# Kernel tuning notes

Hardware: AMD Instinct MI355X
Metric: run time of the kernel (lower is better)

The kernel has to match this reference:

```python
import jax, jax.numpy as jnp
import numpy as np

N = 4096
BATCH = 4
NT = 256  # nt from init_kwargs


def setup_inputs() -> dict:
    key = jax.random.key(0)
    k1, k2, k3, k4 = jax.random.split(key, 4)
    scale = 0.05 / np.sqrt(N)  # keep spectral radius << 1 for numerical stability
    B_real = jax.random.normal(k1, (N, N), dtype=jnp.float32) * scale
    B_imag = jax.random.normal(k2, (N, N), dtype=jnp.float32) * scale
    # omega: per-node frequencies, |omega| <= 0.5 so the diagonal part is contractive
    omega = jax.random.uniform(k3, (BATCH, N), dtype=jnp.float32, minval=-0.5, maxval=0.5)
    # initial state on the unit circle: x0 = exp(i * theta), theta in (-pi, pi)
    x0_angles = jax.random.uniform(k4, (BATCH, N), dtype=jnp.float32, minval=-np.pi, maxval=np.pi)
    return {"B_real": B_real, "B_imag": B_imag, "omega": omega, "x0_angles": x0_angles}


def reference(B_real, B_imag, omega, x0_angles):
    B = B_real + 1j * B_imag            # (N, N) complex64
    x0 = jnp.exp(1j * x0_angles)        # (BATCH, N) complex64, unit-circle init

    def step(x, _):
        # x_{t+1} = i*diag(omega) x_t + B x_t  (batched dense matvec)
        x_next = 1j * omega * x + jnp.einsum('mn,bn->bm', B, x)
        return x_next, x_next

    _, hist = jax.lax.scan(step, x0, None, length=NT - 1)
    # (NT, BATCH, N): initial state followed by NT-1 scan outputs
    return jnp.concatenate([x0[None, ...], hist], axis=0)
```

## Files before the change

kernel.cpp:

```cpp
#include <hip/hip_runtime.h>
#include <stdint.h>

#define NN 4096
#define BB 4
#define MROWS 16
#define TPB 512
#define NBLK 256
#define REDS 17
#define RING 16
#define XSZ  (8 * NN)

typedef __attribute__((ext_vector_type(8))) short bf16x8;
typedef __attribute__((ext_vector_type(4))) float f32x4;

__device__ __forceinline__ uint32_t bf16rne(float f) {
  uint32_t u = __float_as_uint(f);
  return (u + 0x7FFFu + ((u >> 16) & 1u)) >> 16;
}

__global__ void pack_planes(const float* __restrict__ Br, const float* __restrict__ Bi,
                            uint4* __restrict__ Brb, uint4* __restrict__ Bib) {
  int i = blockIdx.x * blockDim.x + threadIdx.x;
  const float4* r4 = reinterpret_cast<const float4*>(Br) + (size_t)i * 2;
  const float4* m4 = reinterpret_cast<const float4*>(Bi) + (size_t)i * 2;
  float4 a0 = r4[0], a1 = r4[1];
  float4 b0 = m4[0], b1 = m4[1];
  uint4 o;
  o.x = bf16rne(a0.x) | (bf16rne(a0.y) << 16);
  o.y = bf16rne(a0.z) | (bf16rne(a0.w) << 16);
  o.z = bf16rne(a1.x) | (bf16rne(a1.y) << 16);
  o.w = bf16rne(a1.z) | (bf16rne(a1.w) << 16);
  Brb[i] = o;
  o.x = bf16rne(b0.x) | (bf16rne(b0.y) << 16);
  o.y = bf16rne(b0.z) | (bf16rne(b0.w) << 16);
  o.z = bf16rne(b1.x) | (bf16rne(b1.y) << 16);
  o.w = bf16rne(b1.z) | (bf16rne(b1.w) << 16);
  Bib[i] = o;
}

__global__ __launch_bounds__(TPB)
void rnn_persistent(const uint16_t* __restrict__ Brb,
                    const uint16_t* __restrict__ Bib,
                    const float* __restrict__ omega,
                    const float* __restrict__ ang,
                    uint16_t* __restrict__ xring,
                    uint32_t* __restrict__ flags,
                    float* __restrict__ out,
                    int NT) {
  extern __shared__ char smem[];
  uint4* BrL = (uint4*)smem;
  float* red = (float*)(smem + 131072);

  const int tid  = threadIdx.x;
  const int w    = tid >> 6;
  const int lane = tid & 63;
  const int al   = lane & 15;
  const int kq   = lane >> 4;
  const int row0 = blockIdx.x * MROWS;
  const int bid  = blockIdx.x;
  const int p1   = al & 7;
  const int p2   = p1 ^ 1;
  const int swz  = al & 7;
  const uint64_t sm64 = (al & 1) ? 0ull : 0x8000800080008000ull;

  for (int j = tid; j < MROWS * 512; j += TPB) {
    int row = j >> 9;
    int u   = j & 511;
    uint4 v = *(const uint4*)(Brb + (size_t)(row0 + row) * NN + u * 8);
    BrL[row * 512 + (u ^ (row & 7))] = v;
  }

  float myval = 0.f, om = 0.f;
  int bb = 0, mm = 0, ri = 0, cc = 0;
  if (tid < 128) {
    int r = tid >> 3; cc = tid & 7;
    mm = row0 + r; bb = cc >> 1; ri = cc & 1;
    om = omega[bb * NN + mm];
    float sv, cv;
    sincosf(ang[bb * NN + mm], &sv, &cv);
    myval = ri ? sv : cv;
    if (!ri) out[bb * NN + mm] = myval;
    float s2 = __shfl(myval, (lane + 8) & 63, 64);
    if (!((tid >> 3) & 1)) {
      uint32_t pk = bf16rne(myval) | (bf16rne(s2) << 16);
      uint32_t* dst = (uint32_t*)xring + ((cc * NN + mm) >> 1);
      __hip_atomic_store(dst, pk, __ATOMIC_RELAXED, __HIP_MEMORY_SCOPE_AGENT);
    }
  }
  __syncthreads();
  if (tid == 0)
    __hip_atomic_store(&flags[bid * 16], 1u, __ATOMIC_RELAXED, __HIP_MEMORY_SCOPE_AGENT);

  const int nb = w * 512 + kq * 8;
  const uint16_t* birow = Bib + (size_t)(row0 + al) * NN + nb;

  for (int t = 1; t < NT; ++t) {
    if (tid < 64) {
      const uint32_t want = (uint32_t)t;
      bool done = false;
      for (int spin = 0; spin < (1 << 22) && !done; ++spin) {
        bool ok = true;
#pragma unroll
        for (int i = 0; i < 4; ++i) {
          uint32_t f = __hip_atomic_load(&flags[(lane * 4 + i) * 16],
                                         __ATOMIC_RELAXED, __HIP_MEMORY_SCOPE_AGENT);
          ok &= (f >= want);
        }
        done = (bool)__all(ok);
        if (!done) __builtin_amdgcn_s_sleep(2);
      }
    }
    __syncthreads();

    const uint16_t* xs = xring + (size_t)((t - 1) & (RING - 1)) * XSZ;
    f32x4 accA = {0.f, 0.f, 0.f, 0.f};
    f32x4 accB = {0.f, 0.f, 0.f, 0.f};

#define SSTEP(S)                                                                \
    { union { uint4 q; bf16x8 v; } fr;                                         \
      fr.q = BrL[al * 512 + (((w << 6) + (S << 2) + kq) ^ swz)];                \
      bf16x8 fi = *(const bf16x8*)(birow + S * 32);                            \
      const uint16_t* x1p = xs + p1 * NN + nb + S * 32;                         \
      const uint16_t* x2p = xs + p2 * NN + nb + S * 32;                         \
      union { uint64_t q[2]; bf16x8 v; } u1, u2;                                \
      u1.q[0] = *(const uint64_t*)(x1p);                                        \
      u1.q[1] = *(const uint64_t*)(x1p + 4);                                    \
      u2.q[0] = *(const uint64_t*)(x2p) ^ sm64;                                 \
      u2.q[1] = *(const uint64_t*)(x2p + 4) ^ sm64;                             \
      accA = __builtin_amdgcn_mfma_f32_16x16x32_bf16(fr.v, u1.v, accA, 0, 0, 0);\
      accB = __builtin_amdgcn_mfma_f32_16x16x32_bf16(fi, u2.v, accB, 0, 0, 0); }
    SSTEP(0)  SSTEP(1)  SSTEP(2)  SSTEP(3)
    SSTEP(4)  SSTEP(5)  SSTEP(6)  SSTEP(7)
    SSTEP(8)  SSTEP(9)  SSTEP(10) SSTEP(11)
    SSTEP(12) SSTEP(13) SSTEP(14) SSTEP(15)
#undef SSTEP

    {
      float* rw = red + w * 16 * REDS;
      rw[(kq * 4 + 0) * REDS + al] = accA[0] + accB[0];
      rw[(kq * 4 + 1) * REDS + al] = accA[1] + accB[1];
      rw[(kq * 4 + 2) * REDS + al] = accA[2] + accB[2];
      rw[(kq * 4 + 3) * REDS + al] = accA[3] + accB[3];
    }
    __syncthreads();

    if (tid < 128) {
      int r = tid >> 3;
      float s = 0.f;
#pragma unroll
      for (int w2 = 0; w2 < 8; ++w2) s += red[w2 * 16 * REDS + r * REDS + cc];
      float other = __shfl_xor(myval, 1, 64);
      float xr = ri ? other : myval;
      float xi = ri ? myval : other;
      s += ri ? (om * xr) : (-om * xi);
      myval = s;
      if (!ri) out[(size_t)t * (BB * NN) + bb * NN + mm] = s;
      float s2 = __shfl(s, (lane + 8) & 63, 64);
      if (!((tid >> 3) & 1)) {
        uint32_t pk = bf16rne(s) | (bf16rne(s2) << 16);
        uint32_t* dst = (uint32_t*)(xring + (size_t)(t & (RING - 1)) * XSZ)
                        + ((cc * NN + mm) >> 1);
        __hip_atomic_store(dst, pk, __ATOMIC_RELAXED, __HIP_MEMORY_SCOPE_AGENT);
      }
    }
    __syncthreads();
    if (tid == 0)
      __hip_atomic_store(&flags[bid * 16], (uint32_t)(t + 1),
                         __ATOMIC_RELAXED, __HIP_MEMORY_SCOPE_AGENT);
  }
}

__global__ void init_kernel(const float* __restrict__ ang,
                            float2* __restrict__ st0, float* __restrict__ out0) {
  int i = blockIdx.x * blockDim.x + threadIdx.x;
  if (i < BB * NN) {
    float s, c;
    sincosf(ang[i], &s, &c);
    st0[i] = make_float2(c, s);
    out0[i] = c;
  }
}

__global__ __launch_bounds__(1024)
void step_fb(const float* __restrict__ Brf, const float* __restrict__ Bif,
             const float* __restrict__ omega,
             const float2* __restrict__ stPrev, float2* __restrict__ stNext,
             float* __restrict__ outRe) {
  extern __shared__ float lds[];
  float* xl  = lds;
  float* xh  = lds + NN * 4;
  float* red = lds + NN * 8;
  const int tid = threadIdx.x;
#pragma unroll
  for (int k = 0; k < 8; ++k) {
    int idx = tid + k * 1024;
    int half = idx >> 12;
    int n = idx & (NN - 1);
    float2 v0 = stPrev[(half * 2) * NN + n];
    float2 v1 = stPrev[(half * 2 + 1) * NN + n];
    reinterpret_cast<float4*>(half ? xh : xl)[n] = make_float4(v0.x, v0.y, v1.x, v1.y);
  }
  __syncthreads();
  const int w = tid >> 6, lane = tid & 63, rg = w >> 2, q = w & 3;
  const int row0 = blockIdx.x * MROWS + rg * 4;
  float acc[4][8];
#pragma unroll
  for (int r = 0; r < 4; ++r)
#pragma unroll
    for (int c = 0; c < 8; ++c) acc[r][c] = 0.0f;
#define CFMA(A, BR, BI, XA, XB)                                   \
  A[0] = fmaf(BR, XA.x, A[0]); A[0] = fmaf(-BI, XA.y, A[0]);      \
  A[1] = fmaf(BR, XA.y, A[1]); A[1] = fmaf(BI, XA.x, A[1]);       \
  A[2] = fmaf(BR, XA.z, A[2]); A[2] = fmaf(-BI, XA.w, A[2]);      \
  A[3] = fmaf(BR, XA.w, A[3]); A[3] = fmaf(BI, XA.z, A[3]);       \
  A[4] = fmaf(BR, XB.x, A[4]); A[4] = fmaf(-BI, XB.y, A[4]);      \
  A[5] = fmaf(BR, XB.y, A[5]); A[5] = fmaf(BI, XB.x, A[5]);       \
  A[6] = fmaf(BR, XB.z, A[6]); A[6] = fmaf(-BI, XB.w, A[6]);      \
  A[7] = fmaf(BR, XB.w, A[7]); A[7] = fmaf(BI, XB.z, A[7]);
  for (int i4 = 0; i4 < 4; ++i4) {
    const int n0 = q * 1024 + i4 * 256 + lane * 4;
    float4 xa[4], xb[4];
#pragma unroll
    for (int j = 0; j < 4; ++j) {
      xa[j] = reinterpret_cast<const float4*>(xl)[n0 + j];
      xb[j] = reinterpret_cast<const float4*>(xh)[n0 + j];
    }
#pragma unroll
    for (int r = 0; r < 4; ++r) {
      const float4 pvr = reinterpret_cast<const float4*>(Brf + (size_t)(row0 + r) * NN)[q * 256 + i4 * 64 + lane];
      const float4 pvi = reinterpret_cast<const float4*>(Bif + (size_t)(row0 + r) * NN)[q * 256 + i4 * 64 + lane];
      float* a = acc[r];
      CFMA(a, pvr.x, pvi.x, xa[0], xb[0]);
      CFMA(a, pvr.y, pvi.y, xa[1], xb[1]);
      CFMA(a, pvr.z, pvi.z, xa[2], xb[2]);
      CFMA(a, pvr.w, pvi.w, xa[3], xb[3]);
    }
  }
#undef CFMA
  float t0 = acc[0][0], t1 = acc[0][1], t2 = acc[0][2], t3 = acc[0][3];
  float t4 = acc[0][4], t5 = acc[0][5], t6 = acc[0][6], t7 = acc[0][7];
  float t8 = acc[1][0], t9 = acc[1][1], t10 = acc[1][2], t11 = acc[1][3];
  float t12 = acc[1][4], t13 = acc[1][5], t14 = acc[1][6], t15 = acc[1][7];
  float t16 = acc[2][0], t17 = acc[2][1], t18 = acc[2][2], t19 = acc[2][3];
  float t20 = acc[2][4], t21 = acc[2][5], t22 = acc[2][6], t23 = acc[2][7];
  float t24 = acc[3][0], t25 = acc[3][1], t26 = acc[3][2], t27 = acc[3][3];
  float t28 = acc[3][4], t29 = acc[3][5], t30 = acc[3][6], t31 = acc[3][7];
#define RSTEP(LO, HI, M)                                          \
  { float s_ = up ? LO : HI;                                      \
    s_ = __shfl_xor(s_, M, 64);                                   \
    LO = (up ? HI : LO) + s_; }
  { const bool up = (lane & 32) != 0;
    RSTEP(t0, t16, 32)  RSTEP(t1, t17, 32)  RSTEP(t2, t18, 32)  RSTEP(t3, t19, 32)
    RSTEP(t4, t20, 32)  RSTEP(t5, t21, 32)  RSTEP(t6, t22, 32)  RSTEP(t7, t23, 32)
    RSTEP(t8, t24, 32)  RSTEP(t9, t25, 32)  RSTEP(t10, t26, 32) RSTEP(t11, t27, 32)
    RSTEP(t12, t28, 32) RSTEP(t13, t29, 32) RSTEP(t14, t30, 32) RSTEP(t15, t31, 32) }
  { const bool up = (lane & 16) != 0;
    RSTEP(t0, t8, 16)  RSTEP(t1, t9, 16)  RSTEP(t2, t10, 16) RSTEP(t3, t11, 16)
    RSTEP(t4, t12, 16) RSTEP(t5, t13, 16) RSTEP(t6, t14, 16) RSTEP(t7, t15, 16) }
  { const bool up = (lane & 8) != 0;
    RSTEP(t0, t4, 8) RSTEP(t1, t5, 8) RSTEP(t2, t6, 8) RSTEP(t3, t7, 8) }
  { const bool up = (lane & 4) != 0;
    RSTEP(t0, t2, 4) RSTEP(t1, t3, 4) }
  { const bool up = (lane & 2) != 0;
    RSTEP(t0, t1, 2) }
#undef RSTEP
  t0 += __shfl_xor(t0, 1, 64);
  if (!(lane & 1)) red[w * 32 + ((lane >> 1) & 31)] = t0;
  __syncthreads();
  if (tid < 128) {
    int rg2 = tid >> 5, v = tid & 31;
    float s = red[(rg2 * 4 + 0) * 32 + v] + red[(rg2 * 4 + 1) * 32 + v] +
              red[(rg2 * 4 + 2) * 32 + v] + red[(rg2 * 4 + 3) * 32 + v];
    int r = v >> 3, c = v & 7, b = c >> 1, ri = c & 1;
    int m = blockIdx.x * MROWS + rg2 * 4 + r;
    float om = omega[b * NN + m];
    const float* xs = (b < 2) ? xl : xh;
    float xr = xs[m * 4 + (b & 1) * 2];
    float xi = xs[m * 4 + (b & 1) * 2 + 1];
    s += (ri == 0) ? (-om * xi) : (om * xr);
    reinterpret_cast<float*>(stNext)[(b * NN + m) * 2 + ri] = s;
    if (ri == 0) outRe[b * NN + m] = s;
  }
}

extern "C" void kernel_launch(void* const* d_in, const int* in_sizes, int n_in,
                              void* d_out, int out_size, void* d_ws, size_t ws_size,
                              hipStream_t stream) {
  const float* B_real = (const float*)d_in[0];
  const float* B_imag = (const float*)d_in[1];
  const float* omega  = (const float*)d_in[2];
  const float* ang    = (const float*)d_in[3];
  float* out = (float*)d_out;

  int NT = out_size / (BB * NN);
  const size_t planeBytes = (size_t)NN * NN * 2;
  const size_t xringBytes = (size_t)RING * XSZ * 2;
  const size_t flagBytes  = 256 * 16 * sizeof(uint32_t);
  const bool coop = ws_size >= 2 * planeBytes + xringBytes + flagBytes;

  hipError_t launched = hipErrorUnknown;
  if (coop) {
    uint16_t* Brb   = (uint16_t*)d_ws;
    uint16_t* Bib   = Brb + (size_t)NN * NN;
    uint16_t* xring = (uint16_t*)((char*)d_ws + 2 * planeBytes);
    uint32_t* flags = (uint32_t*)((char*)d_ws + 2 * planeBytes + xringBytes);

    (void)hipMemsetAsync((void*)flags, 0, flagBytes, stream);
    pack_planes<<<NN * NN / 8 / 256, 256, 0, stream>>>(B_real, B_imag,
                                                       (uint4*)Brb, (uint4*)Bib);

    const size_t shmem = 131072 + (size_t)8 * 16 * REDS * 4;
    (void)hipFuncSetAttribute((const void*)&rnn_persistent,
                              hipFuncAttributeMaxDynamicSharedMemorySize, (int)shmem);

    void* kargs[8];
    kargs[0] = (void*)&Brb;
    kargs[1] = (void*)&Bib;
    kargs[2] = (void*)&omega;
    kargs[3] = (void*)&ang;
    kargs[4] = (void*)&xring;
    kargs[5] = (void*)&flags;
    kargs[6] = (void*)&out;
    kargs[7] = (void*)&NT;
    launched = hipLaunchCooperativeKernel((const void*)&rnn_persistent,
                                          dim3(NBLK), dim3(TPB),
                                          kargs, (unsigned int)shmem, stream);
  }

  if (launched != hipSuccess) {
    float2* st0 = (float2*)d_ws;
    float2* st1 = st0 + BB * NN;
    const size_t shmemF = (size_t)(NN * 8 + 16 * 32) * sizeof(float);
    (void)hipFuncSetAttribute((const void*)&step_fb,
                              hipFuncAttributeMaxDynamicSharedMemorySize, (int)shmemF);
    init_kernel<<<(BB * NN + 255) / 256, 256, 0, stream>>>(ang, st0, out);
    for (int t = 1; t < NT; ++t) {
      float2* sp = ((t - 1) & 1) ? st1 : st0;
      float2* sn = (t & 1) ? st1 : st0;
      float* outT = out + (size_t)t * BB * NN;
      step_fb<<<NN / MROWS, 1024, shmemF, stream>>>(B_real, B_imag, omega, sp, sn, outT);
    }
  }
}
```

Measured before the change: 2.363 ms.

## Replace all-to-all flag polling with master-block barrier and epoch broadcast

Per-step grid synchronization changes from every block polling all 256 per-block flags to a two-level scheme. Block 0 waits on all flags, one thread per flag, then publishes an epoch counter, and every other block spins on that single word with one thread. Flags are padded to 128-byte spacing. The aim is to cut global polling traffic and contention on the flag lines, at the cost of an extra serialized hop (gather, then broadcast) in every step's barrier latency.

```diff
diff --git a/kernel.cpp b/kernel.cpp
--- a/kernel.cpp
+++ b/kernel.cpp
@@ -9,6 +9,7 @@
 #define REDS 17
 #define RING 16
 #define XSZ  (8 * NN)
+#define EPOCH_OFF (256 * 32)
 
 typedef __attribute__((ext_vector_type(8))) short bf16x8;
 typedef __attribute__((ext_vector_type(4))) float f32x4;
@@ -89,28 +90,38 @@
   }
   __syncthreads();
   if (tid == 0)
-    __hip_atomic_store(&flags[bid * 16], 1u, __ATOMIC_RELAXED, __HIP_MEMORY_SCOPE_AGENT);
+    __hip_atomic_store(&flags[bid * 32], 1u, __ATOMIC_RELAXED, __HIP_MEMORY_SCOPE_AGENT);
 
   const int nb = w * 512 + kq * 8;
   const uint16_t* birow = Bib + (size_t)(row0 + al) * NN + nb;
 
   for (int t = 1; t < NT; ++t) {
-    if (tid < 64) {
-      const uint32_t want = (uint32_t)t;
-      bool done = false;
-      for (int spin = 0; spin < (1 << 22) && !done; ++spin) {
-        bool ok = true;
-#pragma unroll
-        for (int i = 0; i < 4; ++i) {
-          uint32_t f = __hip_atomic_load(&flags[(lane * 4 + i) * 16],
+    if (bid == 0) {
+      if (tid < 256) {
+        const uint32_t want = (uint32_t)t;
+        for (int spin = 0; spin < (1 << 22); ++spin) {
+          uint32_t f = __hip_atomic_load(&flags[tid * 32],
                                          __ATOMIC_RELAXED, __HIP_MEMORY_SCOPE_AGENT);
-          ok &= (f >= want);
+          if (f >= want) break;
+          __builtin_amdgcn_s_sleep(1);
         }
-        done = (bool)__all(ok);
-        if (!done) __builtin_amdgcn_s_sleep(2);
       }
-    }
-    __syncthreads();
+      __syncthreads();
+      if (tid == 0)
+        __hip_atomic_store(&flags[EPOCH_OFF], (uint32_t)t,
+                           __ATOMIC_RELAXED, __HIP_MEMORY_SCOPE_AGENT);
+    } else {
+      if (tid == 0) {
+        const uint32_t want = (uint32_t)t;
+        for (int spin = 0; spin < (1 << 22); ++spin) {
+          uint32_t e = __hip_atomic_load(&flags[EPOCH_OFF],
+                                         __ATOMIC_RELAXED, __HIP_MEMORY_SCOPE_AGENT);
+          if (e >= want) break;
+          __builtin_amdgcn_s_sleep(1);
+        }
+      }
+      __syncthreads();
+    }
 
     const uint16_t* xs = xring + (size_t)((t - 1) & (RING - 1)) * XSZ;
     f32x4 accA = {0.f, 0.f, 0.f, 0.f};
@@ -165,7 +176,7 @@
     }
     __syncthreads();
     if (tid == 0)
-      __hip_atomic_store(&flags[bid * 16], (uint32_t)(t + 1),
+      __hip_atomic_store(&flags[bid * 32], (uint32_t)(t + 1),
                          __ATOMIC_RELAXED, __HIP_MEMORY_SCOPE_AGENT);
   }
 }
@@ -295,7 +306,7 @@
   int NT = out_size / (BB * NN);
   const size_t planeBytes = (size_t)NN * NN * 2;
   const size_t xringBytes = (size_t)RING * XSZ * 2;
-  const size_t flagBytes  = 256 * 16 * sizeof(uint32_t);
+  const size_t flagBytes  = (256 * 32 + 32) * sizeof(uint32_t);
   const bool coop = ws_size >= 2 * planeBytes + xringBytes + flagBytes;
 
   hipError_t launched = hipErrorUnknown;
```

New measurement: 2.364 ms. About the same (+0.1%).

## Replace per-step flag barrier with sentinel-valued data polling in x ring

Applied to the files above, without the earlier changes.

Drops the global flag array and the all-blocks spin barrier, and instead marks ring slots with an all-ones sentinel that consumers poll on while loading the previous state directly. Each block re-poisons its own slice of the ring slot from three steps back. This removes a full grid-wide barrier round trip per timestep and lets loads overlap with the wait. The risk is that the ordering is relaxed with no fence between data and sentinel reset, and a genuine bf16 pair could equal the sentinel (NaN pattern). It also adds a launch_bounds occupancy hint of 2 blocks per CU.

```diff
diff --git a/kernel.cpp b/kernel.cpp
--- a/kernel.cpp
+++ b/kernel.cpp
@@ -38,13 +38,17 @@
   Bib[i] = o;
 }
 
-__global__ __launch_bounds__(TPB)
+#define AL64(p)  __hip_atomic_load((const unsigned long long*)(p), \
+                                   __ATOMIC_RELAXED, __HIP_MEMORY_SCOPE_AGENT)
+#define AST32(p, v) __hip_atomic_store((uint32_t*)(p), (v), \
+                                       __ATOMIC_RELAXED, __HIP_MEMORY_SCOPE_AGENT)
+
+__global__ __launch_bounds__(TPB, 2)
 void rnn_persistent(const uint16_t* __restrict__ Brb,
                     const uint16_t* __restrict__ Bib,
                     const float* __restrict__ omega,
                     const float* __restrict__ ang,
                     uint16_t* __restrict__ xring,
-                    uint32_t* __restrict__ flags,
                     float* __restrict__ out,
                     int NT) {
   extern __shared__ char smem[];
@@ -57,7 +61,6 @@
   const int al   = lane & 15;
   const int kq   = lane >> 4;
   const int row0 = blockIdx.x * MROWS;
-  const int bid  = blockIdx.x;
   const int p1   = al & 7;
   const int p2   = p1 ^ 1;
   const int swz  = al & 7;
@@ -83,57 +86,53 @@
     float s2 = __shfl(myval, (lane + 8) & 63, 64);
     if (!((tid >> 3) & 1)) {
       uint32_t pk = bf16rne(myval) | (bf16rne(s2) << 16);
-      uint32_t* dst = (uint32_t*)xring + ((cc * NN + mm) >> 1);
-      __hip_atomic_store(dst, pk, __ATOMIC_RELAXED, __HIP_MEMORY_SCOPE_AGENT);
+      AST32((uint32_t*)xring + ((cc * NN + mm) >> 1), pk);
     }
   }
   __syncthreads();
-  if (tid == 0)
-    __hip_atomic_store(&flags[bid * 16], 1u, __ATOMIC_RELAXED, __HIP_MEMORY_SCOPE_AGENT);
 
   const int nb = w * 512 + kq * 8;
   const uint16_t* birow = Bib + (size_t)(row0 + al) * NN + nb;
 
+#define GDECL(S) unsigned long long gA##S##0, gA##S##1, gB##S##0, gB##S##1;
+#define GISS(S)  gA##S##0 = AL64(xp1 + (S)*32);     gA##S##1 = AL64(xp1 + (S)*32 + 4); \
+                 gB##S##0 = AL64(xp2 + (S)*32);     gB##S##1 = AL64(xp2 + (S)*32 + 4);
+#define VERW(v, p) { int sp_ = 0; \
+    while (((uint32_t)(v) == 0xFFFFFFFFu || (uint32_t)((v) >> 32) == 0xFFFFFFFFu) \
+           && sp_ < (1 << 22)) { (v) = AL64(p); ++sp_; } }
+#define GVER(S) VERW(gA##S##0, xp1 + (S)*32) VERW(gA##S##1, xp1 + (S)*32 + 4) \
+                VERW(gB##S##0, xp2 + (S)*32) VERW(gB##S##1, xp2 + (S)*32 + 4)
+#define SSTEPG(S) { union { uint4 q; bf16x8 v; } fr; \
+      fr.q = BrL[al * 512 + (((w << 6) + ((S) << 2) + kq) ^ swz)]; \
+      bf16x8 fi = *(const bf16x8*)(birow + (S) * 32); \
+      union { unsigned long long q[2]; bf16x8 v; } u1, u2; \
+      u1.q[0] = gA##S##0;        u1.q[1] = gA##S##1; \
+      u2.q[0] = gB##S##0 ^ sm64; u2.q[1] = gB##S##1 ^ sm64; \
+      accA = __builtin_amdgcn_mfma_f32_16x16x32_bf16(fr.v, u1.v, accA, 0, 0, 0); \
+      accB = __builtin_amdgcn_mfma_f32_16x16x32_bf16(fi,   u2.v, accB, 0, 0, 0); }
+
   for (int t = 1; t < NT; ++t) {
-    if (tid < 64) {
-      const uint32_t want = (uint32_t)t;
-      bool done = false;
-      for (int spin = 0; spin < (1 << 22) && !done; ++spin) {
-        bool ok = true;
-#pragma unroll
-        for (int i = 0; i < 4; ++i) {
-          uint32_t f = __hip_atomic_load(&flags[(lane * 4 + i) * 16],
-                                         __ATOMIC_RELAXED, __HIP_MEMORY_SCOPE_AGENT);
-          ok &= (f >= want);
-        }
-        done = (bool)__all(ok);
-        if (!done) __builtin_amdgcn_s_sleep(2);
-      }
-    }
-    __syncthreads();
-
-    const uint16_t* xs = xring + (size_t)((t - 1) & (RING - 1)) * XSZ;
+    const uint16_t* xs  = xring + (size_t)((t - 1) & (RING - 1)) * XSZ;
+    const uint16_t* xp1 = xs + p1 * NN + nb;
+    const uint16_t* xp2 = xs + p2 * NN + nb;
+
     f32x4 accA = {0.f, 0.f, 0.f, 0.f};
     f32x4 accB = {0.f, 0.f, 0.f, 0.f};
 
-#define SSTEP(S)                                                                \
-    { union { uint4 q; bf16x8 v; } fr;                                         \
-      fr.q = BrL[al * 512 + (((w << 6) + (S << 2) + kq) ^ swz)];                \
-      bf16x8 fi = *(const bf16x8*)(birow + S * 32);                            \
-      const uint16_t* x1p = xs + p1 * NN + nb + S * 32;                         \
-      const uint16_t* x2p = xs + p2 * NN + nb + S * 32;                         \
-      union { uint64_t q[2]; bf16x8 v; } u1, u2;                                \
-      u1.q[0] = *(const uint64_t*)(x1p);                                        \
-      u1.q[1] = *(const uint64_t*)(x1p + 4);                                    \
-      u2.q[0] = *(const uint64_t*)(x2p) ^ sm64;                                 \
-      u2.q[1] = *(const uint64_t*)(x2p + 4) ^ sm64;                             \
-      accA = __builtin_amdgcn_mfma_f32_16x16x32_bf16(fr.v, u1.v, accA, 0, 0, 0);\
-      accB = __builtin_amdgcn_mfma_f32_16x16x32_bf16(fi, u2.v, accB, 0, 0, 0); }
-    SSTEP(0)  SSTEP(1)  SSTEP(2)  SSTEP(3)
-    SSTEP(4)  SSTEP(5)  SSTEP(6)  SSTEP(7)
-    SSTEP(8)  SSTEP(9)  SSTEP(10) SSTEP(11)
-    SSTEP(12) SSTEP(13) SSTEP(14) SSTEP(15)
-#undef SSTEP
+    GDECL(0)  GDECL(1)  GDECL(2)  GDECL(3)
+    GDECL(4)  GDECL(5)  GDECL(6)  GDECL(7)
+    GDECL(8)  GDECL(9)  GDECL(10) GDECL(11)
+    GDECL(12) GDECL(13) GDECL(14) GDECL(15)
+
+    GISS(0)  GISS(1)  GISS(2)  GISS(3)  GISS(4)  GISS(5)  GISS(6)  GISS(7)
+    GISS(8)  GISS(9)  GISS(10) GISS(11) GISS(12) GISS(13) GISS(14) GISS(15)
+
+    GVER(0) GVER(1) GVER(2) GVER(3) GVER(4) GVER(5) GVER(6) GVER(7)
+    SSTEPG(0) SSTEPG(1) SSTEPG(2) SSTEPG(3)
+    SSTEPG(4) SSTEPG(5) SSTEPG(6) SSTEPG(7)
+    GVER(8) GVER(9) GVER(10) GVER(11) GVER(12) GVER(13) GVER(14) GVER(15)
+    SSTEPG(8)  SSTEPG(9)  SSTEPG(10) SSTEPG(11)
+    SSTEPG(12) SSTEPG(13) SSTEPG(14) SSTEPG(15)
 
     {
       float* rw = red + w * 16 * REDS;
@@ -158,16 +157,23 @@
       float s2 = __shfl(s, (lane + 8) & 63, 64);
       if (!((tid >> 3) & 1)) {
         uint32_t pk = bf16rne(s) | (bf16rne(s2) << 16);
-        uint32_t* dst = (uint32_t*)(xring + (size_t)(t & (RING - 1)) * XSZ)
-                        + ((cc * NN + mm) >> 1);
-        __hip_atomic_store(dst, pk, __ATOMIC_RELAXED, __HIP_MEMORY_SCOPE_AGENT);
+        AST32((uint32_t*)(xring + (size_t)(t & (RING - 1)) * XSZ)
+              + ((cc * NN + mm) >> 1), pk);
       }
     }
+
+    if (t >= 3 && tid < 64) {
+      uint32_t* pb = (uint32_t*)(xring + (size_t)((t - 3) & (RING - 1)) * XSZ);
+      int c = tid >> 3, k = tid & 7;
+      AST32(pb + c * (NN / 2) + (row0 >> 1) + k, 0xFFFFFFFFu);
+    }
     __syncthreads();
-    if (tid == 0)
-      __hip_atomic_store(&flags[bid * 16], (uint32_t)(t + 1),
-                         __ATOMIC_RELAXED, __HIP_MEMORY_SCOPE_AGENT);
-  }
+  }
+#undef SSTEPG
+#undef GVER
+#undef VERW
+#undef GISS
+#undef GDECL
 }
 
 __global__ void init_kernel(const float* __restrict__ ang,
@@ -295,17 +301,15 @@
   int NT = out_size / (BB * NN);
   const size_t planeBytes = (size_t)NN * NN * 2;
   const size_t xringBytes = (size_t)RING * XSZ * 2;
-  const size_t flagBytes  = 256 * 16 * sizeof(uint32_t);
-  const bool coop = ws_size >= 2 * planeBytes + xringBytes + flagBytes;
+  const bool coop = ws_size >= 2 * planeBytes + xringBytes;
 
   hipError_t launched = hipErrorUnknown;
   if (coop) {
     uint16_t* Brb   = (uint16_t*)d_ws;
     uint16_t* Bib   = Brb + (size_t)NN * NN;
     uint16_t* xring = (uint16_t*)((char*)d_ws + 2 * planeBytes);
-    uint32_t* flags = (uint32_t*)((char*)d_ws + 2 * planeBytes + xringBytes);
-
-    (void)hipMemsetAsync((void*)flags, 0, flagBytes, stream);
+
+    (void)hipMemsetAsync((void*)xring, 0xFF, xringBytes, stream);
     pack_planes<<<NN * NN / 8 / 256, 256, 0, stream>>>(B_real, B_imag,
                                                        (uint4*)Brb, (uint4*)Bib);
 
@@ -313,15 +317,14 @@
     (void)hipFuncSetAttribute((const void*)&rnn_persistent,
                               hipFuncAttributeMaxDynamicSharedMemorySize, (int)shmem);
 
-    void* kargs[8];
+    void* kargs[7];
     kargs[0] = (void*)&Brb;
     kargs[1] = (void*)&Bib;
     kargs[2] = (void*)&omega;
     kargs[3] = (void*)&ang;
     kargs[4] = (void*)&xring;
-    kargs[5] = (void*)&flags;
-    kargs[6] = (void*)&out;
-    kargs[7] = (void*)&NT;
+    kargs[5] = (void*)&out;
+    kargs[6] = (void*)&NT;
     launched = hipLaunchCooperativeKernel((const void*)&rnn_persistent,
                                           dim3(NBLK), dim3(TPB),
                                           kargs, (unsigned int)shmem, stream);
```

Measured after the change: 6.762 ms. +186.2%, slower.
